# Kernel tuning notes

Hardware: AMD Instinct MI355X
Metric: run time of the kernel (lower is better)

The kernel has to match this reference:

```python
import jax, jax.numpy as jnp
import numpy as np

N, E = 50000, 800000          # nodes, edges (avg degree 16)
D_IN, D_H, D_OUT = 128, 128, 64
BN_EPS = 1e-5


def setup_inputs() -> dict:
    key = jax.random.key(0)
    ks = jax.random.split(key, 8)
    g = lambda k, shp, s: jax.random.normal(k, shp, jnp.float32) * s
    return {
        "x": jax.random.normal(ks[0], (N, D_IN), jnp.float32),
        "edge_index": jax.random.randint(ks[1], (2, E), 0, N),
        # SAGEConv layer 1: lin_l (neighbors, with bias), lin_r (root, no bias)
        "Wl1": g(ks[2], (D_IN, D_H), 0.05),
        "Wr1": g(ks[3], (D_IN, D_H), 0.05),
        "b1": jnp.zeros((D_H,), jnp.float32),
        # BatchNorm1d(hidden)
        "gamma": jnp.ones((D_H,), jnp.float32),
        "beta": jnp.zeros((D_H,), jnp.float32),
        # SAGEConv layer 2
        "Wl2": g(ks[4], (D_H, D_OUT), 0.05),
        "Wr2": g(ks[5], (D_H, D_OUT), 0.05),
        "b2": jnp.zeros((D_OUT,), jnp.float32),
    }


def _sage_conv(x, src, dst, Wl, Wr, b):
    """PyG SAGEConv (mean aggr): lin_l(mean_{j in N(i)} x_j) + lin_r(x_i)."""
    n = x.shape[0]
    agg = jax.ops.segment_sum(x[src], dst, num_segments=n)            # [N, d]
    cnt = jax.ops.segment_sum(jnp.ones((src.shape[0],), x.dtype), dst,
                              num_segments=n)                          # [N]
    agg = agg / jnp.maximum(cnt, 1.0)[:, None]                         # mean, 0 for isolated
    return agg @ Wl + x @ Wr + b


def _batch_norm(x, gamma, beta):
    """Training-mode BatchNorm1d: batch stats over the node axis, biased var."""
    mu = jnp.mean(x, axis=0)
    var = jnp.var(x, axis=0)
    return gamma * (x - mu) * jax.lax.rsqrt(var + BN_EPS) + beta


def reference(x, edge_index, Wl1, Wr1, b1, gamma, beta, Wl2, Wr2, b2):
    src, dst = edge_index[0], edge_index[1]
    h = _sage_conv(x, src, dst, Wl1, Wr1, b1)
    h = jax.nn.relu(_batch_norm(h, gamma, beta))
    # dropout is identity in eval / deterministic reference
    return _sage_conv(h, src, dst, Wl2, Wr2, b2)
```

## Files before the change

kernel.cpp:

```cpp
#include <hip/hip_runtime.h>
#include <hip/hip_bf16.h>
#include <hip/hip_fp8.h>

#define DIN   128
#define DH    128
#define DOUTC 64
#define BN_EPS 1e-5f

typedef __attribute__((ext_vector_type(8))) short bf16x8;
typedef __attribute__((ext_vector_type(4))) float f32x4;
typedef __attribute__((ext_vector_type(2))) float f32x2;

#ifndef __has_builtin
#define __has_builtin(x) 0
#endif
#if __has_builtin(__builtin_amdgcn_cvt_pk_f32_fp8) && __has_builtin(__builtin_amdgcn_cvt_pk_fp8_f32)
#define HW_FP8 1
#else
#define HW_FP8 0
#endif

__device__ inline unsigned short f2bf(float f) {
    __hip_bfloat16 b = __float2bfloat16(f);
    return *reinterpret_cast<unsigned short*>(&b);
}
__device__ inline float bf2f(unsigned short u) {
    return __uint_as_float(((unsigned int)u) << 16);
}
__device__ inline void fp8x4_to_f32(unsigned int w, float* o) {
#if HW_FP8
    f32x2 lo = __builtin_amdgcn_cvt_pk_f32_fp8((int)w, false);
    f32x2 hi = __builtin_amdgcn_cvt_pk_f32_fp8((int)w, true);
    o[0] = lo.x; o[1] = lo.y; o[2] = hi.x; o[3] = hi.y;
#else
    #pragma unroll
    for (int c = 0; c < 4; ++c) {
        __hip_fp8_e4m3 q; q.__x = (__hip_fp8_storage_t)((w >> (8 * c)) & 0xFF);
        o[c] = (float)q;
    }
#endif
}
__device__ inline unsigned int f32x4_to_fp8(float a, float b, float c, float d) {
#if HW_FP8
    int p = __builtin_amdgcn_cvt_pk_fp8_f32(a, b, 0, false);
    p = __builtin_amdgcn_cvt_pk_fp8_f32(c, d, p, true);
    return (unsigned int)p;
#else
    __hip_fp8_e4m3 qa(a), qb(b), qc(c), qd(d);
    return (unsigned int)qa.__x | ((unsigned int)qb.__x << 8) |
           ((unsigned int)qc.__x << 16) | ((unsigned int)qd.__x << 24);
#endif
}

__device__ inline void block_excl_scan_256(const int* __restrict__ arr,
                                           int* __restrict__ excl,
                                           int* __restrict__ wsum, int tid)
{
    int lane = tid & 63, w = tid >> 6;
    int v = arr[tid];
    int inc = v;
    #pragma unroll
    for (int off = 1; off < 64; off <<= 1) {
        int t = __shfl_up(inc, off, 64);
        if (lane >= off) inc += t;
    }
    if (lane == 63) wsum[w] = inc;
    __syncthreads();
    if (tid == 0) {
        int s = 0;
        #pragma unroll
        for (int i = 0; i < 4; ++i) { int t = wsum[i]; wsum[i] = s; s += t; }
    }
    __syncthreads();
    excl[tid] = inc - v + wsum[w];
    __syncthreads();
}

__global__ __launch_bounds__(256) void prep_kernel(
    const float* __restrict__ x, unsigned char* __restrict__ xq,
    const float* __restrict__ Wl1, const float* __restrict__ Wr1,
    const float* __restrict__ Wl2, const float* __restrict__ Wr2,
    unsigned short* __restrict__ W1p, unsigned short* __restrict__ W2p,
    const int* __restrict__ ei, int* __restrict__ cursor,
    unsigned int* __restrict__ coarse,
    int total8, int cvtB, int E, int nb, int cap)
{
    __shared__ int hist[256], lstart[256], gbase[256], wsum[4];
    __shared__ unsigned int staged[4096];
    const int b = blockIdx.x;
    const int tid = threadIdx.x;

    if (b < cvtB) {
        int i = b * 256 + tid;
        if (i >= total8) return;
        float4 a = ((const float4*)x)[2 * i];
        float4 c = ((const float4*)x)[2 * i + 1];
        uint2 pk;
        pk.x = f32x4_to_fp8(a.x, a.y, a.z, a.w);
        pk.y = f32x4_to_fp8(c.x, c.y, c.z, c.w);
        *(uint2*)(xq + (size_t)i * 8) = pk;
        return;
    }
    if (b < cvtB + 192) {
        int region = (b - cvtB) >> 6;
        int idx = ((b - cvtB) & 63) * 256 + tid;
        int k = idx >> 7, c = idx & 127;
        int d = ((k >> 5) * 8 + (c >> 4)) * 512 + ((k >> 3) & 3) * 128 + (c & 15) * 8 + (k & 7);
        if (region == 0)      W1p[d] = f2bf(Wl1[idx]);
        else if (region == 1) W1p[128 * 128 + d] = f2bf(Wr1[idx]);
        else {
            float v = (c < 64) ? Wl2[k * 64 + c] : Wr2[k * 64 + (c - 64)];
            W2p[d] = f2bf(v);
        }
        return;
    }

    const int chunkBase = (b - cvtB - 192) * 4096;
    hist[tid] = 0;
    __syncthreads();

    unsigned int rec[16]; int pos[16]; int bb[16];
    #pragma unroll
    for (int i = 0; i < 16; ++i) {
        int e = chunkBase + i * 256 + tid;
        if (e < E) {
            int s = ei[e], d = ei[E + e];
            rec[i] = ((unsigned int)d << 16) | (unsigned int)s;
            bb[i]  = d >> 8;
            pos[i] = atomicAdd(&hist[bb[i]], 1);
        } else bb[i] = -1;
    }
    __syncthreads();

    block_excl_scan_256(hist, lstart, wsum, tid);

    if (tid < nb) {
        int c = hist[tid];
        gbase[tid] = c ? atomicAdd(&cursor[tid], c) : 0;
    }
    __syncthreads();

    #pragma unroll
    for (int i = 0; i < 16; ++i)
        if (bb[i] >= 0) staged[lstart[bb[i]] + pos[i]] = rec[i];
    __syncthreads();

    int total = min(4096, E - chunkBase);
    for (int i = tid; i < total; i += 256) {
        unsigned int r = staged[i];
        int bk  = (int)(r >> 24);
        int gp  = gbase[bk] + (i - lstart[bk]);
        if (gp < cap) coarse[(size_t)bk * cap + gp] = r;
    }
}

__global__ __launch_bounds__(256) void bin_fine(
    const int* __restrict__ cursor, const unsigned int* __restrict__ coarse,
    unsigned short* __restrict__ sorted, int* __restrict__ deg,
    int* __restrict__ row_start, int n, int cap)
{
    __shared__ int hist[256], pstart[256], cur2[256], wsum[4];
    const int b = blockIdx.x, tid = threadIdx.x;
    const int cnt = min(cursor[b], cap);
    const unsigned int* src = coarse + (size_t)b * cap;

    hist[tid] = 0;
    __syncthreads();

    int nIter = (cnt + 255) >> 8;
    for (int i = 0; i < nIter; ++i) {
        int idx = i * 256 + tid;
        if (idx < cnt) atomicAdd(&hist[(src[idx] >> 16) & 255], 1);
    }
    __syncthreads();

    block_excl_scan_256(hist, pstart, wsum, tid);
    cur2[tid] = pstart[tid];
    __syncthreads();

    for (int i = 0; i < nIter; ++i) {
        int idx = i * 256 + tid;
        if (idx < cnt) {
            unsigned int r = src[idx];
            int dl = (r >> 16) & 255;
            int p  = atomicAdd(&cur2[dl], 1);
            sorted[(size_t)b * cap + p] = (unsigned short)(r & 0xFFFFu);
        }
    }

    int node = b * 256 + tid;
    if (node < n) {
        deg[node]       = hist[tid];
        row_start[node] = b * cap + pstart[tid];
    }
}

__global__ __launch_bounds__(256) void gemm1_fused(
    const unsigned char* __restrict__ xq, const float* __restrict__ x,
    const int* __restrict__ row_start, const int* __restrict__ deg,
    const unsigned short* __restrict__ sorted,
    const unsigned short* __restrict__ W1p, const float* __restrict__ bias,
    unsigned short* __restrict__ hb,
    float* __restrict__ bn_part, int nblk, int n)
{
    __shared__ unsigned short G[32][136];
    __shared__ float red[2][2][128];

    const int block_row = blockIdx.x * 32;
    const int tid  = threadIdx.x;
    const int wave = tid >> 6;
    const int lane = tid & 63;
    const int q    = lane >> 4;
    const int m16  = lane & 15;
    const int rg   = wave >> 1;
    const int ch   = wave & 1;

    {
        int sub = lane & 7, oct = lane >> 3;
        int lr = rg * 16 + ch * 8 + oct;
        int g  = block_row + lr;
        float acc[16];
        #pragma unroll
        for (int j = 0; j < 16; ++j) acc[j] = 0.f;
        int d = 0, base = 0;
        if (g < n) { base = row_start[g]; d = deg[g]; }
        int nb8 = (d + 7) >> 3;
        int si[8];
        if (nb8 > 0) {
            #pragma unroll
            for (int u = 0; u < 8; ++u)
                si[u] = (int)sorted[base + (u < d ? u : 0)];
        }
        for (int b = 0; b < nb8; ++b) {
            uint4 raws[8];
            #pragma unroll
            for (int u = 0; u < 8; ++u)
                raws[u] = ((const uint4*)(xq + (size_t)si[u] * DIN))[sub];
            if (b + 1 < nb8) {
                int t0n = (b + 1) * 8;
                #pragma unroll
                for (int u = 0; u < 8; ++u) {
                    int tt = t0n + u;
                    si[u] = (int)sorted[base + (tt < d ? tt : 0)];
                }
            }
            int t0 = b * 8;
            #pragma unroll
            for (int u = 0; u < 8; ++u) {
                float w8 = (t0 + u < d) ? 1.0f : 0.0f;
                const unsigned int* w = (const unsigned int*)&raws[u];
                #pragma unroll
                for (int c = 0; c < 4; ++c) {
                    float o4[4];
                    fp8x4_to_f32(w[c], o4);
                    acc[c*4+0] = fmaf(o4[0], w8, acc[c*4+0]);
                    acc[c*4+1] = fmaf(o4[1], w8, acc[c*4+1]);
                    acc[c*4+2] = fmaf(o4[2], w8, acc[c*4+2]);
                    acc[c*4+3] = fmaf(o4[3], w8, acc[c*4+3]);
                }
            }
        }
        float inv = 1.0f / fmaxf((float)d, 1.0f);
        unsigned short t16[16];
        #pragma unroll
        for (int j = 0; j < 16; ++j) t16[j] = f2bf(acc[j] * inv);
        *(uint4*)&G[lr][sub * 16]     = ((uint4*)t16)[0];
        *(uint4*)&G[lr][sub * 16 + 8] = ((uint4*)t16)[1];
    }
    __syncthreads();

    f32x4 acc[4];
    #pragma unroll
    for (int nt = 0; nt < 4; ++nt) acc[nt] = (f32x4){0.f, 0.f, 0.f, 0.f};

    const int grow = block_row + rg * 16 + m16;
    #pragma unroll
    for (int ks = 0; ks < 4; ++ks) {
        bf16x8 ag = *(const bf16x8*)&G[rg * 16 + m16][ks * 32 + q * 8];
        const unsigned short* wp0 = W1p + (size_t)ks * 8 * 512 + (size_t)ch * 4 * 512;
        #pragma unroll
        for (int nt = 0; nt < 4; ++nt) {
            bf16x8 b = *(const bf16x8*)(wp0 + nt * 512 + lane * 8);
            acc[nt] = __builtin_amdgcn_mfma_f32_16x16x32_bf16(ag, b, acc[nt], 0, 0, 0);
        }
        bf16x8 ax;
        {
            float4 f0 = {0.f,0.f,0.f,0.f}, f1 = {0.f,0.f,0.f,0.f};
            if (grow < n) {
                const float* xr = x + (size_t)grow * DIN + ks * 32 + q * 8;
                f0 = *(const float4*)xr;
                f1 = *(const float4*)(xr + 4);
            }
            unsigned short t[8];
            t[0]=f2bf(f0.x); t[1]=f2bf(f0.y); t[2]=f2bf(f0.z); t[3]=f2bf(f0.w);
            t[4]=f2bf(f1.x); t[5]=f2bf(f1.y); t[6]=f2bf(f1.z); t[7]=f2bf(f1.w);
            ax = *(bf16x8*)t;
        }
        const unsigned short* wp1 = W1p + (size_t)(4 + ks) * 8 * 512 + (size_t)ch * 4 * 512;
        #pragma unroll
        for (int nt = 0; nt < 4; ++nt) {
            bf16x8 b = *(const bf16x8*)(wp1 + nt * 512 + lane * 8);
            acc[nt] = __builtin_amdgcn_mfma_f32_16x16x32_bf16(ax, b, acc[nt], 0, 0, 0);
        }
    }

    float psum[4], psq[4];
    #pragma unroll
    for (int nt = 0; nt < 4; ++nt) {
        int col = (ch * 4 + nt) * 16 + m16;
        float bv = bias[col];
        float s = 0.f, ssq = 0.f;
        #pragma unroll
        for (int reg = 0; reg < 4; ++reg) {
            int g = block_row + rg * 16 + q * 4 + reg;
            float v = acc[nt][reg] + bv;
            if (g < n) {
                hb[(size_t)g * DH + col] = f2bf(v);
                s += v; ssq += v * v;
            }
        }
        psum[nt] = s; psq[nt] = ssq;
    }
    #pragma unroll
    for (int nt = 0; nt < 4; ++nt) {
        psum[nt] += __shfl_xor(psum[nt], 16, 64);
        psum[nt] += __shfl_xor(psum[nt], 32, 64);
        psq[nt]  += __shfl_xor(psq[nt], 16, 64);
        psq[nt]  += __shfl_xor(psq[nt], 32, 64);
    }
    if (lane < 16) {
        #pragma unroll
        for (int nt = 0; nt < 4; ++nt) {
            red[0][rg][(ch * 4 + nt) * 16 + lane] = psum[nt];
            red[1][rg][(ch * 4 + nt) * 16 + lane] = psq[nt];
        }
    }
    __syncthreads();
    if (tid < 128) {
        float s   = red[0][0][tid] + red[0][1][tid];
        float ssq = red[1][0][tid] + red[1][1][tid];
        bn_part[(size_t)tid * nblk + blockIdx.x]         = s;
        bn_part[(size_t)(128 + tid) * nblk + blockIdx.x] = ssq;
    }
}

__global__ __launch_bounds__(256) void bn_reduce(
    const float* __restrict__ bn_part,
    float* __restrict__ bn_sum, float* __restrict__ bn_sumsq, int nblk)
{
    __shared__ float ws[4];
    const int c = blockIdx.x;
    const int tid = threadIdx.x;
    const float* p = bn_part + (size_t)c * nblk;
    float s = 0.f;
    for (int i = tid; i < nblk; i += 256) s += p[i];
    #pragma unroll
    for (int off = 1; off < 64; off <<= 1) s += __shfl_xor(s, off, 64);
    if ((tid & 63) == 0) ws[tid >> 6] = s;
    __syncthreads();
    if (tid == 0) {
        float t = ws[0] + ws[1] + ws[2] + ws[3];
        if (c < 128) bn_sum[c] = t;
        else         bn_sumsq[c - 128] = t;
    }
}

__global__ __launch_bounds__(256) void gemm2p_mfma(
    const unsigned short* __restrict__ hb,
    const float* __restrict__ bn_sum, const float* __restrict__ bn_sumsq,
    const float* __restrict__ gamma, const float* __restrict__ beta,
    const unsigned short* __restrict__ W2p, const float* __restrict__ bias,
    unsigned short* __restrict__ P, float* __restrict__ out, int n)
{
    __shared__ float s_scale[128], s_shift[128];

    const int block_row = blockIdx.x * 64;
    const int tid  = threadIdx.x;
    const int wave = tid >> 6;
    const int lane = tid & 63;
    const int q    = lane >> 4;
    const int m16  = lane & 15;

    if (tid < 128) {
        float invN = 1.0f / (float)n;
        float mu  = bn_sum[tid] * invN;
        float var = bn_sumsq[tid] * invN - mu * mu;
        float sc  = gamma[tid] * rsqrtf(var + BN_EPS);
        s_scale[tid] = sc;
        s_shift[tid] = beta[tid] - mu * sc;
    }
    __syncthreads();

    f32x4 acc[8];
    #pragma unroll
    for (int nt = 0; nt < 8; ++nt) acc[nt] = (f32x4){0.f, 0.f, 0.f, 0.f};

    const int grow = block_row + wave * 16 + m16;
    #pragma unroll
    for (int ks = 0; ks < 4; ++ks) {
        bf16x8 a;
        {
            int kbase = ks * 32 + q * 8;
            float4 sc0 = *(const float4*)&s_scale[kbase];
            float4 sc1 = *(const float4*)&s_scale[kbase + 4];
            float4 sh0 = *(const float4*)&s_shift[kbase];
            float4 sh1 = *(const float4*)&s_shift[kbase + 4];
            unsigned short t[8] = {0,0,0,0,0,0,0,0};
            if (grow < n) {
                uint4 raw = *(const uint4*)(hb + (size_t)grow * DH + kbase);
                const unsigned short* u = (const unsigned short*)&raw;
                t[0] = f2bf(fmaxf(bf2f(u[0]) * sc0.x + sh0.x, 0.f));
                t[1] = f2bf(fmaxf(bf2f(u[1]) * sc0.y + sh0.y, 0.f));
                t[2] = f2bf(fmaxf(bf2f(u[2]) * sc0.z + sh0.z, 0.f));
                t[3] = f2bf(fmaxf(bf2f(u[3]) * sc0.w + sh0.w, 0.f));
                t[4] = f2bf(fmaxf(bf2f(u[4]) * sc1.x + sh1.x, 0.f));
                t[5] = f2bf(fmaxf(bf2f(u[5]) * sc1.y + sh1.y, 0.f));
                t[6] = f2bf(fmaxf(bf2f(u[6]) * sc1.z + sh1.z, 0.f));
                t[7] = f2bf(fmaxf(bf2f(u[7]) * sc1.w + sh1.w, 0.f));
            }
            a = *(bf16x8*)t;
        }
        const unsigned short* wp = W2p + (size_t)ks * 8 * 512;
        #pragma unroll
        for (int nt = 0; nt < 8; ++nt) {
            bf16x8 b = *(const bf16x8*)(wp + nt * 512 + lane * 8);
            acc[nt] = __builtin_amdgcn_mfma_f32_16x16x32_bf16(a, b, acc[nt], 0, 0, 0);
        }
    }

    #pragma unroll
    for (int nt = 0; nt < 4; ++nt) {
        int col = nt * 16 + m16;
        #pragma unroll
        for (int reg = 0; reg < 4; ++reg) {
            int g = block_row + wave * 16 + q * 4 + reg;
            if (g < n) P[(size_t)g * DOUTC + col] = f2bf(acc[nt][reg]);
        }
    }
    #pragma unroll
    for (int nt = 4; nt < 8; ++nt) {
        int col = (nt - 4) * 16 + m16;
        float bv = bias[col];
        #pragma unroll
        for (int reg = 0; reg < 4; ++reg) {
            int g = block_row + wave * 16 + q * 4 + reg;
            if (g < n) out[(size_t)g * DOUTC + col] = acc[nt][reg] + bv;
        }
    }
}

__global__ __launch_bounds__(256) void agg_gather64_add(
    const int* __restrict__ row_start, const int* __restrict__ deg,
    const unsigned short* __restrict__ sorted, const unsigned short* __restrict__ P,
    float* __restrict__ out, int n)
{
    int wid  = (blockIdx.x * 256 + threadIdx.x) >> 6;
    int lane = threadIdx.x & 63;
    int sub = lane & 7, oct = lane >> 3;
    int r = wid * 8 + oct;
    if (r >= n) return;

    float acc[8];
    #pragma unroll
    for (int j = 0; j < 8; ++j) acc[j] = 0.f;

    int base = row_start[r];
    int d    = deg[r];
    int nb8  = (d + 7) >> 3;
    int si[8];
    if (nb8 > 0) {
        #pragma unroll
        for (int u = 0; u < 8; ++u)
            si[u] = (int)sorted[base + (u < d ? u : 0)];
    }
    for (int b = 0; b < nb8; ++b) {
        uint4 raws[8];
        #pragma unroll
        for (int u = 0; u < 8; ++u)
            raws[u] = ((const uint4*)(P + (size_t)si[u] * DOUTC))[sub];
        if (b + 1 < nb8) {
            int t0n = (b + 1) * 8;
            #pragma unroll
            for (int u = 0; u < 8; ++u) {
                int tt = t0n + u;
                si[u] = (int)sorted[base + (tt < d ? tt : 0)];
            }
        }
        int t0 = b * 8;
        #pragma unroll
        for (int u = 0; u < 8; ++u) {
            float w8 = (t0 + u < d) ? 1.0f : 0.0f;
            const unsigned short* us = (const unsigned short*)&raws[u];
            #pragma unroll
            for (int j = 0; j < 8; ++j) acc[j] = fmaf(bf2f(us[j]), w8, acc[j]);
        }
    }
    float inv = 1.0f / fmaxf((float)d, 1.0f);
    float* op = out + (size_t)r * DOUTC + sub * 8;
    float4 c0 = *(float4*)op;
    float4 c1 = *((float4*)op + 1);
    c0.x += acc[0] * inv; c0.y += acc[1] * inv;
    c0.z += acc[2] * inv; c0.w += acc[3] * inv;
    c1.x += acc[4] * inv; c1.y += acc[5] * inv;
    c1.z += acc[6] * inv; c1.w += acc[7] * inv;
    *(float4*)op = c0;
    *((float4*)op + 1) = c1;
}

extern "C" void kernel_launch(void* const* d_in, const int* in_sizes, int n_in,
                              void* d_out, int out_size, void* d_ws, size_t ws_size,
                              hipStream_t stream)
{
    const float* x     = (const float*)d_in[0];
    const int*   ei    = (const int*)  d_in[1];
    const float* Wl1   = (const float*)d_in[2];
    const float* Wr1   = (const float*)d_in[3];
    const float* b1    = (const float*)d_in[4];
    const float* gamma = (const float*)d_in[5];
    const float* beta  = (const float*)d_in[6];
    const float* Wl2   = (const float*)d_in[7];
    const float* Wr2   = (const float*)d_in[8];
    const float* b2    = (const float*)d_in[9];
    float*       out   = (float*)d_out;

    const int N = in_sizes[0] / DIN;
    const int E = in_sizes[1] / 2;

    const int NB  = (N + 255) >> 8;
    int cap = (E / NB) * 3 / 2 + 256;
    cap = (cap + 255) & ~255;

    const int gemm1_blocks = (N + 31) / 32;
    const int gemm2_blocks = (N + 63) / 64;

    float* bn_sum   = (float*)d_ws;
    float* bn_sumsq = bn_sum + DH;
    int* cursor     = (int*)(bn_sumsq + DH);
    int* deg        = cursor + 256;
    int* row_start  = deg + N;
    unsigned int* coarse   = (unsigned int*)(row_start + N);
    unsigned short* sorted = (unsigned short*)(coarse + (size_t)NB * cap);
    unsigned short* hb     = sorted + (size_t)NB * cap;
    unsigned short* P      = hb + (size_t)N * DH;
    unsigned short* W1p    = P + (size_t)N * DOUTC;
    unsigned short* W2p    = W1p + 256 * 128;
    unsigned char*  xq     = (unsigned char*)(W2p + 128 * 128);
    float* bn_part  = (float*)(xq + (size_t)N * DIN);

    hipMemsetAsync(bn_sum, 0, (2 * DH + 256) * sizeof(float), stream);

    dim3 blk(256);
    const int cvtB        = (N * DIN / 8 + 255) / 256;
    const int binA_blocks = (E + 4095) / 4096;
    const int g64_blocks  = ((N + 7) / 8 + 3) / 4;

    prep_kernel<<<cvtB + 192 + binA_blocks, blk, 0, stream>>>(
        x, xq, Wl1, Wr1, Wl2, Wr2, W1p, W2p,
        ei, cursor, coarse, N * DIN / 8, cvtB, E, NB, cap);

    bin_fine<<<NB, blk, 0, stream>>>(cursor, coarse, sorted, deg, row_start, N, cap);

    gemm1_fused<<<gemm1_blocks, blk, 0, stream>>>(xq, x, row_start, deg, sorted,
                                                  W1p, b1, hb, bn_part, gemm1_blocks, N);

    bn_reduce<<<256, blk, 0, stream>>>(bn_part, bn_sum, bn_sumsq, gemm1_blocks);

    gemm2p_mfma<<<gemm2_blocks, blk, 0, stream>>>(hb, bn_sum, bn_sumsq,
                                                  gamma, beta, W2p, b2, P, out, N);

    agg_gather64_add<<<g64_blocks, blk, 0, stream>>>(row_start, deg, sorted,
                                                     P, out, N);
}
```

Baseline: 188.0 us.

## Replace two-pass CSR binning with fixed-capacity per-node adjacency via global atomics

```diff
diff --git a/kernel.cpp b/kernel.cpp
--- a/kernel.cpp
+++ b/kernel.cpp
@@ -6,6 +6,7 @@
 #define DH    128
 #define DOUTC 64
 #define BN_EPS 1e-5f
+#define DEGCAP 64
 
 typedef __attribute__((ext_vector_type(8))) short bf16x8;
 typedef __attribute__((ext_vector_type(4))) float f32x4;
@@ -52,41 +53,15 @@
 #endif
 }
 
-__device__ inline void block_excl_scan_256(const int* __restrict__ arr,
-                                           int* __restrict__ excl,
-                                           int* __restrict__ wsum, int tid)
-{
-    int lane = tid & 63, w = tid >> 6;
-    int v = arr[tid];
-    int inc = v;
-    #pragma unroll
-    for (int off = 1; off < 64; off <<= 1) {
-        int t = __shfl_up(inc, off, 64);
-        if (lane >= off) inc += t;
-    }
-    if (lane == 63) wsum[w] = inc;
-    __syncthreads();
-    if (tid == 0) {
-        int s = 0;
-        #pragma unroll
-        for (int i = 0; i < 4; ++i) { int t = wsum[i]; wsum[i] = s; s += t; }
-    }
-    __syncthreads();
-    excl[tid] = inc - v + wsum[w];
-    __syncthreads();
-}
-
 __global__ __launch_bounds__(256) void prep_kernel(
     const float* __restrict__ x, unsigned char* __restrict__ xq,
     const float* __restrict__ Wl1, const float* __restrict__ Wr1,
     const float* __restrict__ Wl2, const float* __restrict__ Wr2,
     unsigned short* __restrict__ W1p, unsigned short* __restrict__ W2p,
-    const int* __restrict__ ei, int* __restrict__ cursor,
-    unsigned int* __restrict__ coarse,
-    int total8, int cvtB, int E, int nb, int cap)
-{
-    __shared__ int hist[256], lstart[256], gbase[256], wsum[4];
-    __shared__ unsigned int staged[4096];
+    const int* __restrict__ ei, int* __restrict__ deg,
+    unsigned short* __restrict__ sorted,
+    int total8, int cvtB, int E)
+{
     const int b = blockIdx.x;
     const int tid = threadIdx.x;
 
@@ -116,92 +91,23 @@
     }
 
     const int chunkBase = (b - cvtB - 192) * 4096;
-    hist[tid] = 0;
-    __syncthreads();
-
-    unsigned int rec[16]; int pos[16]; int bb[16];
     #pragma unroll
     for (int i = 0; i < 16; ++i) {
         int e = chunkBase + i * 256 + tid;
         if (e < E) {
             int s = ei[e], d = ei[E + e];
-            rec[i] = ((unsigned int)d << 16) | (unsigned int)s;
-            bb[i]  = d >> 8;
-            pos[i] = atomicAdd(&hist[bb[i]], 1);
-        } else bb[i] = -1;
-    }
-    __syncthreads();
-
-    block_excl_scan_256(hist, lstart, wsum, tid);
-
-    if (tid < nb) {
-        int c = hist[tid];
-        gbase[tid] = c ? atomicAdd(&cursor[tid], c) : 0;
-    }
-    __syncthreads();
-
-    #pragma unroll
-    for (int i = 0; i < 16; ++i)
-        if (bb[i] >= 0) staged[lstart[bb[i]] + pos[i]] = rec[i];
-    __syncthreads();
-
-    int total = min(4096, E - chunkBase);
-    for (int i = tid; i < total; i += 256) {
-        unsigned int r = staged[i];
-        int bk  = (int)(r >> 24);
-        int gp  = gbase[bk] + (i - lstart[bk]);
-        if (gp < cap) coarse[(size_t)bk * cap + gp] = r;
-    }
-}
-
-__global__ __launch_bounds__(256) void bin_fine(
-    const int* __restrict__ cursor, const unsigned int* __restrict__ coarse,
-    unsigned short* __restrict__ sorted, int* __restrict__ deg,
-    int* __restrict__ row_start, int n, int cap)
-{
-    __shared__ int hist[256], pstart[256], cur2[256], wsum[4];
-    const int b = blockIdx.x, tid = threadIdx.x;
-    const int cnt = min(cursor[b], cap);
-    const unsigned int* src = coarse + (size_t)b * cap;
-
-    hist[tid] = 0;
-    __syncthreads();
-
-    int nIter = (cnt + 255) >> 8;
-    for (int i = 0; i < nIter; ++i) {
-        int idx = i * 256 + tid;
-        if (idx < cnt) atomicAdd(&hist[(src[idx] >> 16) & 255], 1);
-    }
-    __syncthreads();
-
-    block_excl_scan_256(hist, pstart, wsum, tid);
-    cur2[tid] = pstart[tid];
-    __syncthreads();
-
-    for (int i = 0; i < nIter; ++i) {
-        int idx = i * 256 + tid;
-        if (idx < cnt) {
-            unsigned int r = src[idx];
-            int dl = (r >> 16) & 255;
-            int p  = atomicAdd(&cur2[dl], 1);
-            sorted[(size_t)b * cap + p] = (unsigned short)(r & 0xFFFFu);
-        }
-    }
-
-    int node = b * 256 + tid;
-    if (node < n) {
-        deg[node]       = hist[tid];
-        row_start[node] = b * cap + pstart[tid];
+            int p = atomicAdd(&deg[d], 1);
+            if (p < DEGCAP) sorted[(size_t)d * DEGCAP + p] = (unsigned short)s;
+        }
     }
 }
 
 __global__ __launch_bounds__(256) void gemm1_fused(
     const unsigned char* __restrict__ xq, const float* __restrict__ x,
-    const int* __restrict__ row_start, const int* __restrict__ deg,
-    const unsigned short* __restrict__ sorted,
+    const int* __restrict__ deg, const unsigned short* __restrict__ sorted,
     const unsigned short* __restrict__ W1p, const float* __restrict__ bias,
     unsigned short* __restrict__ hb,
-    float* __restrict__ bn_part, int nblk, int n)
+    float* __restrict__ bn_part, int n)
 {
     __shared__ unsigned short G[32][136];
     __shared__ float red[2][2][128];
@@ -223,13 +129,14 @@
         #pragma unroll
         for (int j = 0; j < 16; ++j) acc[j] = 0.f;
         int d = 0, base = 0;
-        if (g < n) { base = row_start[g]; d = deg[g]; }
-        int nb8 = (d + 7) >> 3;
+        if (g < n) { d = deg[g]; base = g * DEGCAP; }
+        int dl = d < DEGCAP ? d : DEGCAP;
+        int nb8 = (dl + 7) >> 3;
         int si[8];
         if (nb8 > 0) {
             #pragma unroll
             for (int u = 0; u < 8; ++u)
-                si[u] = (int)sorted[base + (u < d ? u : 0)];
+                si[u] = (int)sorted[base + (u < dl ? u : 0)];
         }
         for (int b = 0; b < nb8; ++b) {
             uint4 raws[8];
@@ -241,13 +148,13 @@
                 #pragma unroll
                 for (int u = 0; u < 8; ++u) {
                     int tt = t0n + u;
-                    si[u] = (int)sorted[base + (tt < d ? tt : 0)];
+                    si[u] = (int)sorted[base + (tt < dl ? tt : 0)];
                 }
             }
             int t0 = b * 8;
             #pragma unroll
             for (int u = 0; u < 8; ++u) {
-                float w8 = (t0 + u < d) ? 1.0f : 0.0f;
+                float w8 = (t0 + u < dl) ? 1.0f : 0.0f;
                 const unsigned int* w = (const unsigned int*)&raws[u];
                 #pragma unroll
                 for (int c = 0; c < 4; ++c) {
@@ -339,30 +246,19 @@
     if (tid < 128) {
         float s   = red[0][0][tid] + red[0][1][tid];
         float ssq = red[1][0][tid] + red[1][1][tid];
-        bn_part[(size_t)tid * nblk + blockIdx.x]         = s;
-        bn_part[(size_t)(128 + tid) * nblk + blockIdx.x] = ssq;
+        bn_part[(size_t)blockIdx.x * 256 + tid]       = s;
+        bn_part[(size_t)blockIdx.x * 256 + 128 + tid] = ssq;
     }
 }
 
 __global__ __launch_bounds__(256) void bn_reduce(
-    const float* __restrict__ bn_part,
-    float* __restrict__ bn_sum, float* __restrict__ bn_sumsq, int nblk)
-{
-    __shared__ float ws[4];
-    const int c = blockIdx.x;
+    const float* __restrict__ bn_part, float* __restrict__ bn_out, int nblk)
+{
     const int tid = threadIdx.x;
-    const float* p = bn_part + (size_t)c * nblk;
     float s = 0.f;
-    for (int i = tid; i < nblk; i += 256) s += p[i];
-    #pragma unroll
-    for (int off = 1; off < 64; off <<= 1) s += __shfl_xor(s, off, 64);
-    if ((tid & 63) == 0) ws[tid >> 6] = s;
-    __syncthreads();
-    if (tid == 0) {
-        float t = ws[0] + ws[1] + ws[2] + ws[3];
-        if (c < 128) bn_sum[c] = t;
-        else         bn_sumsq[c - 128] = t;
-    }
+    for (int r = blockIdx.x; r < nblk; r += 64)
+        s += bn_part[(size_t)r * 256 + tid];
+    atomicAdd(&bn_out[tid], s);
 }
 
 __global__ __launch_bounds__(256) void gemm2p_mfma(
@@ -450,8 +346,8 @@
 }
 
 __global__ __launch_bounds__(256) void agg_gather64_add(
-    const int* __restrict__ row_start, const int* __restrict__ deg,
-    const unsigned short* __restrict__ sorted, const unsigned short* __restrict__ P,
+    const int* __restrict__ deg, const unsigned short* __restrict__ sorted,
+    const unsigned short* __restrict__ P,
     float* __restrict__ out, int n)
 {
     int wid  = (blockIdx.x * 256 + threadIdx.x) >> 6;
@@ -464,14 +360,15 @@
     #pragma unroll
     for (int j = 0; j < 8; ++j) acc[j] = 0.f;
 
-    int base = row_start[r];
     int d    = deg[r];
-    int nb8  = (d + 7) >> 3;
+    int base = r * DEGCAP;
+    int dl   = d < DEGCAP ? d : DEGCAP;
+    int nb8  = (dl + 7) >> 3;
     int si[8];
     if (nb8 > 0) {
         #pragma unroll
         for (int u = 0; u < 8; ++u)
-            si[u] = (int)sorted[base + (u < d ? u : 0)];
+            si[u] = (int)sorted[base + (u < dl ? u : 0)];
     }
     for (int b = 0; b < nb8; ++b) {
         uint4 raws[8];
@@ -483,13 +380,13 @@
             #pragma unroll
             for (int u = 0; u < 8; ++u) {
                 int tt = t0n + u;
-                si[u] = (int)sorted[base + (tt < d ? tt : 0)];
+                si[u] = (int)sorted[base + (tt < dl ? tt : 0)];
             }
         }
         int t0 = b * 8;
         #pragma unroll
         for (int u = 0; u < 8; ++u) {
-            float w8 = (t0 + u < d) ? 1.0f : 0.0f;
+            float w8 = (t0 + u < dl) ? 1.0f : 0.0f;
             const unsigned short* us = (const unsigned short*)&raws[u];
             #pragma unroll
             for (int j = 0; j < 8; ++j) acc[j] = fmaf(bf2f(us[j]), w8, acc[j]);
@@ -526,48 +423,38 @@
     const int N = in_sizes[0] / DIN;
     const int E = in_sizes[1] / 2;
 
-    const int NB  = (N + 255) >> 8;
-    int cap = (E / NB) * 3 / 2 + 256;
-    cap = (cap + 255) & ~255;
-
     const int gemm1_blocks = (N + 31) / 32;
     const int gemm2_blocks = (N + 63) / 64;
 
     float* bn_sum   = (float*)d_ws;
     float* bn_sumsq = bn_sum + DH;
-    int* cursor     = (int*)(bn_sumsq + DH);
-    int* deg        = cursor + 256;
-    int* row_start  = deg + N;
-    unsigned int* coarse   = (unsigned int*)(row_start + N);
-    unsigned short* sorted = (unsigned short*)(coarse + (size_t)NB * cap);
-    unsigned short* hb     = sorted + (size_t)NB * cap;
+    int*   deg      = (int*)(bn_sumsq + DH);
+    unsigned short* sorted = (unsigned short*)(deg + N);
+    unsigned short* hb     = sorted + (size_t)N * DEGCAP;
     unsigned short* P      = hb + (size_t)N * DH;
     unsigned short* W1p    = P + (size_t)N * DOUTC;
     unsigned short* W2p    = W1p + 256 * 128;
     unsigned char*  xq     = (unsigned char*)(W2p + 128 * 128);
     float* bn_part  = (float*)(xq + (size_t)N * DIN);
 
-    hipMemsetAsync(bn_sum, 0, (2 * DH + 256) * sizeof(float), stream);
+    hipMemsetAsync(bn_sum, 0, (size_t)(2 * DH + N) * sizeof(int), stream);
 
     dim3 blk(256);
     const int cvtB        = (N * DIN / 8 + 255) / 256;
-    const int binA_blocks = (E + 4095) / 4096;
+    const int edge_blocks = (E + 4095) / 4096;
     const int g64_blocks  = ((N + 7) / 8 + 3) / 4;
 
-    prep_kernel<<<cvtB + 192 + binA_blocks, blk, 0, stream>>>(
+    prep_kernel<<<cvtB + 192 + edge_blocks, blk, 0, stream>>>(
         x, xq, Wl1, Wr1, Wl2, Wr2, W1p, W2p,
-        ei, cursor, coarse, N * DIN / 8, cvtB, E, NB, cap);
-
-    bin_fine<<<NB, blk, 0, stream>>>(cursor, coarse, sorted, deg, row_start, N, cap);
-
-    gemm1_fused<<<gemm1_blocks, blk, 0, stream>>>(xq, x, row_start, deg, sorted,
-                                                  W1p, b1, hb, bn_part, gemm1_blocks, N);
-
-    bn_reduce<<<256, blk, 0, stream>>>(bn_part, bn_sum, bn_sumsq, gemm1_blocks);
+        ei, deg, sorted, N * DIN / 8, cvtB, E);
+
+    gemm1_fused<<<gemm1_blocks, blk, 0, stream>>>(xq, x, deg, sorted,
+                                                  W1p, b1, hb, bn_part, N);
+
+    bn_reduce<<<64, blk, 0, stream>>>(bn_part, bn_sum, gemm1_blocks);
 
     gemm2p_mfma<<<gemm2_blocks, blk, 0, stream>>>(hb, bn_sum, bn_sumsq,
                                                   gamma, beta, W2p, b2, P, out, N);
 
-    agg_gather64_add<<<g64_blocks, blk, 0, stream>>>(row_start, deg, sorted,
-                                                     P, out, N);
-}
+    agg_gather64_add<<<g64_blocks, blk, 0, stream>>>(deg, sorted, P, out, N);
+}
```

After: 236.7 us. 1.26x slower.
